# Optimization experiments

Measured on AMD Instinct MI355X. Metric: run time of the kernel, lower is better.

Reference implementation:

```python
import jax, jax.numpy as jnp
import numpy as np

ATTN_MULT = 8.0
NEG_INF = float('-inf')

N, Q, S, D = 16, 2048, 2048, 64


def setup_inputs() -> dict:
    key = jax.random.key(0)
    kq, kk, kv, kp = jax.random.split(key, 4)
    return {
        "queries_nqd": jax.random.normal(kq, (N, Q, D), dtype=jnp.float32),
        "keys_nsd": jax.random.normal(kk, (N, S, D), dtype=jnp.float32),
        "values_nsv": jax.random.normal(kv, (N, S, D), dtype=jnp.float32),
        "prefix_len_n": jax.random.randint(kp, (N,), 0, S, dtype=jnp.int64 if jax.config.jax_enable_x64 else jnp.int32),
    }


def reference(queries_nqd, keys_nsd, values_nsv, prefix_len_n):
    # attention_type == 'block_diagonal', backend == 'torch', dropout p == 0
    n, q, d = queries_nqd.shape
    s = keys_nsd.shape[1]
    scale = ATTN_MULT / d
    # prefix-block mask: key position < prefix_len (broadcast over queries)
    block_mask_n1s = (jnp.arange(s)[None, None, :] < prefix_len_n[:, None, None])  # [n,1,s]
    diag_mask_qs = jnp.arange(q)[:, None] == jnp.arange(s)[None, :]                # [q,s]
    mask_nqs = block_mask_n1s | diag_mask_qs[None, :, :]                           # [n,q,s]
    scores_nqs = jnp.einsum('nqd,nsd->nqs', queries_nqd, keys_nsd) * scale
    scores_nqs = jnp.where(mask_nqs, scores_nqs, NEG_INF)
    probs_nqs = jax.nn.softmax(scores_nqs, axis=-1)
    return jnp.einsum('nqs,nsv->nqv', probs_nqs, values_nsv)
```

## Files before the change

kernel.cpp:

```cpp
#include <hip/hip_runtime.h>
#include <math.h>

#define NH 16
#define QL 2048
#define SL 2048
#define DD 64
#define PSTR 72
#define QK_SCALE_LOG2E 0.1803368801111f

typedef __attribute__((ext_vector_type(8))) short short8;
typedef __attribute__((ext_vector_type(4))) float floatx4;
typedef __attribute__((ext_vector_type(4))) unsigned short ushort4v;
typedef __attribute__((ext_vector_type(8))) unsigned short ushort8v;

__device__ __forceinline__ unsigned short f2bf(float x) {
    unsigned u = __float_as_uint(x);
    u += 0x7FFFu + ((u >> 16) & 1u);
    return (unsigned short)(u >> 16);
}

__device__ __forceinline__ void gld16(const unsigned short* g, unsigned short* l) {
    __builtin_amdgcn_global_load_lds(
        (const __attribute__((address_space(1))) unsigned int*)g,
        (__attribute__((address_space(3))) unsigned int*)l, 16, 0, 0);
}

__global__ __launch_bounds__(256) void convqk(
    const float* __restrict__ Qf, const float* __restrict__ Kf,
    unsigned short* __restrict__ Qb, unsigned short* __restrict__ Kb)
{
    int idx = blockIdx.x * 256 + threadIdx.x;
    const float4* src; unsigned short* dst; float scale;
    if (blockIdx.y == 0) { src = (const float4*)Qf; dst = Qb; scale = QK_SCALE_LOG2E; }
    else                 { src = (const float4*)Kf; dst = Kb; scale = 1.0f; }
    float4 v = src[idx];
    ushort4v h = { f2bf(v.x * scale), f2bf(v.y * scale), f2bf(v.z * scale), f2bf(v.w * scale) };
    *(ushort4v*)(dst + (size_t)idx * 4) = h;
}

__global__ __launch_bounds__(256) void transv(
    const float* __restrict__ Vf, unsigned short* __restrict__ Vtb)
{
    __shared__ unsigned short sT[64][PSTR];
    int bx = blockIdx.x;
    int n = bx >> 5, stile = bx & 31, s0 = stile * 64;
    int tid = (int)threadIdx.x;
    const float* vb = Vf + ((size_t)n * SL + s0) * DD;
    #pragma unroll
    for (int i = 0; i < 4; ++i) {
        int idx = tid + i * 256;
        int r = idx >> 4, c = (idx & 15) << 2;
        float4 v = *(const float4*)(vb + r * DD + c);
        sT[c + 0][r] = f2bf(v.x);
        sT[c + 1][r] = f2bf(v.y);
        sT[c + 2][r] = f2bf(v.z);
        sT[c + 3][r] = f2bf(v.w);
    }
    __syncthreads();
    int d = tid >> 2, sg = tid & 3;
    unsigned short* out = Vtb + (size_t)n * DD * SL + (size_t)d * SL + s0 + sg * 16;
    ushort8v a, b;
    #pragma unroll
    for (int i = 0; i < 8; ++i) { a[i] = sT[d][sg * 16 + i]; b[i] = sT[d][sg * 16 + 8 + i]; }
    *(ushort8v*)(out) = a;
    *(ushort8v*)(out + 8) = b;
}

__global__ __launch_bounds__(256, 4) void attn_mfma_split(
    const unsigned short* __restrict__ Qb, const unsigned short* __restrict__ Kb,
    const unsigned short* __restrict__ Vtb, const int* __restrict__ plen_g,
    float* __restrict__ Op, float* __restrict__ Lp, int spl)
{
    __shared__ unsigned short sQ[64 * 64];
    __shared__ unsigned short sK[64 * 64];
    __shared__ unsigned short sVt[64 * 64];
    __shared__ unsigned short sP[4 * 16 * PSTR];

    const int blk = blockIdx.x;
    const int n  = blk & (NH - 1);
    const int qt = blk >> 4;
    const int q0 = qt * 64;
    const int sp = blockIdx.y;
    const int sbeg = sp * spl;
    const int plen = plen_g[n];
    const bool hasdiag = (q0 >= sbeg) && (q0 < sbeg + spl);
    if (!((sbeg < plen) || hasdiag)) return;

    const int tid  = (int)threadIdx.x;
    const int wave = tid >> 6, lane = tid & 63, quad = lane >> 4, l16 = lane & 15;

    {
        const unsigned short* qg = Qb + ((size_t)(n * QL + q0)) * DD;
        #pragma unroll
        for (int j = 0; j < 2; ++j) {
            int seg = wave * 2 + j;
            int r = seg * 8 + (lane >> 3);
            int cg = (lane & 7) ^ (r & 7);
            gld16(qg + r * DD + cg * 8, sQ + seg * 512);
        }
    }

    floatx4 acc[4];
    #pragma unroll
    for (int dt = 0; dt < 4; ++dt) acc[dt] = (floatx4){0.f, 0.f, 0.f, 0.f};
    float lsum = 0.f;

    const int ntile = spl >> 6;
    for (int t = 0; t < ntile; ++t) {
        const int s0 = sbeg + t * 64;
        if (!((s0 < plen) || (s0 == q0))) continue;
        __syncthreads();

        const unsigned short* kg = Kb + ((size_t)(n * SL + s0)) * DD;
        const unsigned short* vg = Vtb + (size_t)n * DD * SL + s0;
        #pragma unroll
        for (int j = 0; j < 2; ++j) {
            int seg = wave * 2 + j;
            int r = seg * 8 + (lane >> 3);
            int cg = (lane & 7) ^ (r & 7);
            gld16(kg + r * DD + cg * 8, sK + seg * 512);
            gld16(vg + (size_t)r * SL + cg * 8, sVt + seg * 512);
        }
        __syncthreads();

        floatx4 sf[4];
        #pragma unroll
        for (int st2 = 0; st2 < 4; ++st2) sf[st2] = (floatx4){0.f, 0.f, 0.f, 0.f};
        #pragma unroll
        for (int ks = 0; ks < 2; ++ks) {
            int qrow = wave * 16 + l16;
            short8 bQ = *(const short8*)(sQ + qrow * 64 + (((ks * 4 + quad) ^ (qrow & 7)) * 8));
            #pragma unroll
            for (int st2 = 0; st2 < 4; ++st2) {
                int krow = st2 * 16 + l16;
                short8 aK = *(const short8*)(sK + krow * 64 + (((ks * 4 + quad) ^ (krow & 7)) * 8));
                sf[st2] = __builtin_amdgcn_mfma_f32_16x16x32_bf16(aK, bQ, sf[st2], 0, 0, 0);
            }
        }

        const int qcol = q0 + wave * 16 + l16;
        unsigned short* pw = sP + (wave * 16 + l16) * PSTR;
        if (s0 + 64 <= plen) {
            #pragma unroll
            for (int st2 = 0; st2 < 4; ++st2) {
                float p0 = exp2f(sf[st2][0]);
                float p1 = exp2f(sf[st2][1]);
                float p2 = exp2f(sf[st2][2]);
                float p3 = exp2f(sf[st2][3]);
                lsum += (p0 + p1) + (p2 + p3);
                ushort4v pk = { f2bf(p0), f2bf(p1), f2bf(p2), f2bf(p3) };
                *(ushort4v*)(pw + st2 * 16 + quad * 4) = pk;
            }
        } else {
            #pragma unroll
            for (int st2 = 0; st2 < 4; ++st2) {
                float p[4];
                #pragma unroll
                for (int r = 0; r < 4; ++r) {
                    int s = s0 + st2 * 16 + quad * 4 + r;
                    bool valid = (s < plen) || (s == qcol);
                    p[r] = exp2f(valid ? sf[st2][r] : -INFINITY);
                    lsum += p[r];
                }
                ushort4v pk = { f2bf(p[0]), f2bf(p[1]), f2bf(p[2]), f2bf(p[3]) };
                *(ushort4v*)(pw + st2 * 16 + quad * 4) = pk;
            }
        }

        #pragma unroll
        for (int ks = 0; ks < 2; ++ks) {
            short8 aP = *(const short8*)(sP + (wave * 16 + l16) * PSTR + ks * 32 + quad * 8);
            #pragma unroll
            for (int dt = 0; dt < 4; ++dt) {
                int vrow = dt * 16 + l16;
                short8 bV = *(const short8*)(sVt + vrow * 64 + (((ks * 4 + quad) ^ (vrow & 7)) * 8));
                acc[dt] = __builtin_amdgcn_mfma_f32_16x16x32_bf16(aP, bV, acc[dt], 0, 0, 0);
            }
        }
    }

    lsum += __shfl_xor(lsum, 16, 64);
    lsum += __shfl_xor(lsum, 32, 64);
    if (quad == 0)
        Lp[((size_t)sp * NH + n) * QL + q0 + wave * 16 + l16] = lsum;

    float* ob = Op + (((size_t)sp * NH + n) * QL + q0) * DD;
    #pragma unroll
    for (int r = 0; r < 4; ++r) {
        int ql = wave * 16 + quad * 4 + r;
        #pragma unroll
        for (int dt = 0; dt < 4; ++dt)
            ob[(size_t)ql * DD + dt * 16 + l16] = acc[dt][r];
    }
}

__global__ __launch_bounds__(256) void combine(
    const float* __restrict__ Op, const float* __restrict__ Lp,
    const int* __restrict__ plen_g, float* __restrict__ Og, int nsplit, int spl)
{
    int idx = blockIdx.x * 256 + (int)threadIdx.x;
    int d4 = idx & 15;
    int q  = (idx >> 4) & (QL - 1);
    int n  = idx >> 15;
    int plen = plen_g[n];
    int spd = q / spl;
    float4 s = {0.f, 0.f, 0.f, 0.f};
    float l = 0.f;
    for (int sp = 0; sp < nsplit; ++sp) {
        if ((sp * spl < plen) || (sp == spd)) {
            const float* ob = Op + (((size_t)sp * NH + n) * QL + q) * DD;
            float4 v = *(const float4*)(ob + d4 * 4);
            s.x += v.x; s.y += v.y; s.z += v.z; s.w += v.w;
            l += Lp[((size_t)sp * NH + n) * QL + q];
        }
    }
    float inv = 1.0f / l;
    float4 o = { s.x * inv, s.y * inv, s.z * inv, s.w * inv };
    *(float4*)(Og + ((size_t)n * QL + q) * DD + d4 * 4) = o;
}

extern "C" void kernel_launch(void* const* d_in, const int* in_sizes, int n_in,
                              void* d_out, int out_size, void* d_ws, size_t ws_size,
                              hipStream_t stream) {
    const float* Qf   = (const float*)d_in[0];
    const float* Kf   = (const float*)d_in[1];
    const float* Vf   = (const float*)d_in[2];
    const int*   plen = (const int*)d_in[3];
    float* Og = (float*)d_out;

    char* ws = (char*)d_ws;
    unsigned short* Qb  = (unsigned short*)(ws);
    unsigned short* Kb  = (unsigned short*)(ws + (4u << 20));
    unsigned short* Vtb = (unsigned short*)(ws + (8u << 20));
    float* Op = (float*)(ws + (12u << 20));

    const size_t op_bytes = (size_t)NH * QL * DD * 4;
    const size_t lp_bytes = (size_t)NH * QL * 4;
    int nsplit = 1;
    if (ws_size >= (12u << 20) + 4 * (op_bytes + lp_bytes)) nsplit = 4;
    else if (ws_size >= (12u << 20) + 2 * (op_bytes + lp_bytes)) nsplit = 2;
    float* Lp = (float*)(ws + (12u << 20) + (size_t)nsplit * op_bytes);
    int spl = SL / nsplit;

    convqk<<<dim3(2048, 2), 256, 0, stream>>>(Qf, Kf, Qb, Kb);
    transv<<<512, 256, 0, stream>>>(Vf, Vtb);
    attn_mfma_split<<<dim3(NH * (QL / 64), nsplit), 256, 0, stream>>>(Qb, Kb, Vtb, plen, Op, Lp, spl);
    combine<<<2048, 256, 0, stream>>>(Op, Lp, plen, Og, nsplit, spl);
}
```

Baseline: 116.7 us.

## Double-buffer K/V tiles with prefetch over a compacted tile list

K and V^T shared-memory tiles are double-buffered so the next tile's global-to-LDS load is issued while the current tile is computed. Only the needed tiles (the prefix tiles plus the diagonal tile) are iterated, which removes one barrier per iteration. Q fragments are hoisted out of the loop and exp2f is swapped for the hardware exp2 builtin. The larger LDS footprint lowers the launch-bounds occupancy target from 4 to 3 blocks, and correctness depends on the async LDS loads completing before the barrier.

```diff
diff --git a/kernel.cpp b/kernel.cpp
--- a/kernel.cpp
+++ b/kernel.cpp
@@ -66,14 +66,14 @@
     *(ushort8v*)(out + 8) = b;
 }
 
-__global__ __launch_bounds__(256, 4) void attn_mfma_split(
+__global__ __launch_bounds__(256, 3) void attn_mfma_split(
     const unsigned short* __restrict__ Qb, const unsigned short* __restrict__ Kb,
     const unsigned short* __restrict__ Vtb, const int* __restrict__ plen_g,
     float* __restrict__ Op, float* __restrict__ Lp, int spl)
 {
     __shared__ unsigned short sQ[64 * 64];
-    __shared__ unsigned short sK[64 * 64];
-    __shared__ unsigned short sVt[64 * 64];
+    __shared__ unsigned short sK[2][64 * 64];
+    __shared__ unsigned short sVt[2][64 * 64];
     __shared__ unsigned short sP[4 * 16 * PSTR];
 
     const int blk = blockIdx.x;
@@ -83,21 +83,36 @@
     const int sp = blockIdx.y;
     const int sbeg = sp * spl;
     const int plen = plen_g[n];
+    const int ntile = spl >> 6;
     const bool hasdiag = (q0 >= sbeg) && (q0 < sbeg + spl);
     if (!((sbeg < plen) || hasdiag)) return;
 
     const int tid  = (int)threadIdx.x;
     const int wave = tid >> 6, lane = tid & 63, quad = lane >> 4, l16 = lane & 15;
 
+    int rem  = plen - sbeg;
+    int base = (rem > 0) ? min((rem + 63) >> 6, ntile) : 0;
+    int td   = hasdiag ? ((q0 - sbeg) >> 6) : -1;
+    int total = base + ((td >= base) ? 1 : 0);
+
+    const unsigned short* kh = Kb  + (size_t)n * SL * DD;
+    const unsigned short* vh = Vtb + (size_t)n * DD * SL;
+
+    const int seg0 = wave * 2, seg1 = wave * 2 + 1;
+    const int r0 = seg0 * 8 + (lane >> 3), r1 = seg1 * 8 + (lane >> 3);
+    const int cg0 = ((lane & 7) ^ (r0 & 7)) * 8, cg1 = ((lane & 7) ^ (r1 & 7)) * 8;
+
     {
         const unsigned short* qg = Qb + ((size_t)(n * QL + q0)) * DD;
-        #pragma unroll
-        for (int j = 0; j < 2; ++j) {
-            int seg = wave * 2 + j;
-            int r = seg * 8 + (lane >> 3);
-            int cg = (lane & 7) ^ (r & 7);
-            gld16(qg + r * DD + cg * 8, sQ + seg * 512);
-        }
+        gld16(qg + r0 * DD + cg0, sQ + seg0 * 512);
+        gld16(qg + r1 * DD + cg1, sQ + seg1 * 512);
+        int t0 = (0 < base) ? 0 : td;
+        const unsigned short* kg = kh + (size_t)(sbeg + t0 * 64) * DD;
+        const unsigned short* vg = vh + (sbeg + t0 * 64);
+        gld16(kg + r0 * DD + cg0, sK[0] + seg0 * 512);
+        gld16(kg + r1 * DD + cg1, sK[0] + seg1 * 512);
+        gld16(vg + (size_t)r0 * SL + cg0, sVt[0] + seg0 * 512);
+        gld16(vg + (size_t)r1 * SL + cg1, sVt[0] + seg1 * 512);
     }
 
     floatx4 acc[4];
@@ -105,48 +120,54 @@
     for (int dt = 0; dt < 4; ++dt) acc[dt] = (floatx4){0.f, 0.f, 0.f, 0.f};
     float lsum = 0.f;
 
-    const int ntile = spl >> 6;
-    for (int t = 0; t < ntile; ++t) {
+    const int qrow = wave * 16 + l16;
+    short8 bQ0, bQ1;
+
+    for (int i = 0; i < total; ++i) {
+        __syncthreads();
+
+        if (i + 1 < total) {
+            int tn = (i + 1 < base) ? (i + 1) : td;
+            const unsigned short* kg = kh + (size_t)(sbeg + tn * 64) * DD;
+            const unsigned short* vg = vh + (sbeg + tn * 64);
+            unsigned short* dk = sK[(i + 1) & 1];
+            unsigned short* dv = sVt[(i + 1) & 1];
+            gld16(kg + r0 * DD + cg0, dk + seg0 * 512);
+            gld16(kg + r1 * DD + cg1, dk + seg1 * 512);
+            gld16(vg + (size_t)r0 * SL + cg0, dv + seg0 * 512);
+            gld16(vg + (size_t)r1 * SL + cg1, dv + seg1 * 512);
+        }
+        if (i == 0) {
+            bQ0 = *(const short8*)(sQ + qrow * 64 + (((0 * 4 + quad) ^ (qrow & 7)) * 8));
+            bQ1 = *(const short8*)(sQ + qrow * 64 + (((1 * 4 + quad) ^ (qrow & 7)) * 8));
+        }
+
+        const unsigned short* sk = sK[i & 1];
+        const unsigned short* sv = sVt[i & 1];
+        const int t  = (i < base) ? i : td;
         const int s0 = sbeg + t * 64;
-        if (!((s0 < plen) || (s0 == q0))) continue;
-        __syncthreads();
-
-        const unsigned short* kg = Kb + ((size_t)(n * SL + s0)) * DD;
-        const unsigned short* vg = Vtb + (size_t)n * DD * SL + s0;
-        #pragma unroll
-        for (int j = 0; j < 2; ++j) {
-            int seg = wave * 2 + j;
-            int r = seg * 8 + (lane >> 3);
-            int cg = (lane & 7) ^ (r & 7);
-            gld16(kg + r * DD + cg * 8, sK + seg * 512);
-            gld16(vg + (size_t)r * SL + cg * 8, sVt + seg * 512);
-        }
-        __syncthreads();
 
         floatx4 sf[4];
         #pragma unroll
         for (int st2 = 0; st2 < 4; ++st2) sf[st2] = (floatx4){0.f, 0.f, 0.f, 0.f};
         #pragma unroll
-        for (int ks = 0; ks < 2; ++ks) {
-            int qrow = wave * 16 + l16;
-            short8 bQ = *(const short8*)(sQ + qrow * 64 + (((ks * 4 + quad) ^ (qrow & 7)) * 8));
-            #pragma unroll
-            for (int st2 = 0; st2 < 4; ++st2) {
-                int krow = st2 * 16 + l16;
-                short8 aK = *(const short8*)(sK + krow * 64 + (((ks * 4 + quad) ^ (krow & 7)) * 8));
-                sf[st2] = __builtin_amdgcn_mfma_f32_16x16x32_bf16(aK, bQ, sf[st2], 0, 0, 0);
-            }
-        }
-
-        const int qcol = q0 + wave * 16 + l16;
-        unsigned short* pw = sP + (wave * 16 + l16) * PSTR;
+        for (int st2 = 0; st2 < 4; ++st2) {
+            int krow = st2 * 16 + l16;
+            short8 aK0 = *(const short8*)(sk + krow * 64 + (((0 * 4 + quad) ^ (krow & 7)) * 8));
+            short8 aK1 = *(const short8*)(sk + krow * 64 + (((1 * 4 + quad) ^ (krow & 7)) * 8));
+            sf[st2] = __builtin_amdgcn_mfma_f32_16x16x32_bf16(aK0, bQ0, sf[st2], 0, 0, 0);
+            sf[st2] = __builtin_amdgcn_mfma_f32_16x16x32_bf16(aK1, bQ1, sf[st2], 0, 0, 0);
+        }
+
+        const int qcol = q0 + qrow;
+        unsigned short* pw = sP + qrow * PSTR;
         if (s0 + 64 <= plen) {
             #pragma unroll
             for (int st2 = 0; st2 < 4; ++st2) {
-                float p0 = exp2f(sf[st2][0]);
-                float p1 = exp2f(sf[st2][1]);
-                float p2 = exp2f(sf[st2][2]);
-                float p3 = exp2f(sf[st2][3]);
+                float p0 = __builtin_amdgcn_exp2f(sf[st2][0]);
+                float p1 = __builtin_amdgcn_exp2f(sf[st2][1]);
+                float p2 = __builtin_amdgcn_exp2f(sf[st2][2]);
+                float p3 = __builtin_amdgcn_exp2f(sf[st2][3]);
                 lsum += (p0 + p1) + (p2 + p3);
                 ushort4v pk = { f2bf(p0), f2bf(p1), f2bf(p2), f2bf(p3) };
                 *(ushort4v*)(pw + st2 * 16 + quad * 4) = pk;
@@ -159,7 +180,7 @@
                 for (int r = 0; r < 4; ++r) {
                     int s = s0 + st2 * 16 + quad * 4 + r;
                     bool valid = (s < plen) || (s == qcol);
-                    p[r] = exp2f(valid ? sf[st2][r] : -INFINITY);
+                    p[r] = __builtin_amdgcn_exp2f(valid ? sf[st2][r] : -INFINITY);
                     lsum += p[r];
                 }
                 ushort4v pk = { f2bf(p[0]), f2bf(p[1]), f2bf(p[2]), f2bf(p[3]) };
@@ -169,11 +190,11 @@
 
         #pragma unroll
         for (int ks = 0; ks < 2; ++ks) {
-            short8 aP = *(const short8*)(sP + (wave * 16 + l16) * PSTR + ks * 32 + quad * 8);
+            short8 aP = *(const short8*)(sP + qrow * PSTR + ks * 32 + quad * 8);
             #pragma unroll
             for (int dt = 0; dt < 4; ++dt) {
                 int vrow = dt * 16 + l16;
-                short8 bV = *(const short8*)(sVt + vrow * 64 + (((ks * 4 + quad) ^ (vrow & 7)) * 8));
+                short8 bV = *(const short8*)(sv + vrow * 64 + (((ks * 4 + quad) ^ (vrow & 7)) * 8));
                 acc[dt] = __builtin_amdgcn_mfma_f32_16x16x32_bf16(aP, bV, acc[dt], 0, 0, 0);
             }
         }
@@ -182,7 +203,7 @@
     lsum += __shfl_xor(lsum, 16, 64);
     lsum += __shfl_xor(lsum, 32, 64);
     if (quad == 0)
-        Lp[((size_t)sp * NH + n) * QL + q0 + wave * 16 + l16] = lsum;
+        Lp[((size_t)sp * NH + n) * QL + q0 + qrow] = lsum;
 
     float* ob = Op + (((size_t)sp * NH + n) * QL + q0) * DD;
     #pragma unroll
```

Measured after the change: 114.6 us. Within noise of the previous version (-1.8%).
